# Kernel tuning notes

Hardware: AMD Instinct MI355X
Metric: run time of the kernel (lower is better)

## Reference

```python
import jax, jax.numpy as jnp
import numpy as np

N, E, IN, H, G = 50000, 800000, 200, 128, 512
L, M = 2, 2
D = H - 1  # Lorentz space dims
EPS = 1e-5


def _l_inner(x, y):
    return -x[..., :1] * y[..., :1] + jnp.sum(x[..., 1:] * y[..., 1:], -1, keepdims=True)


def _proj(x, c):
    s = x[..., 1:]
    t = jnp.sqrt(c + jnp.sum(s * s, -1, keepdims=True))
    return jnp.concatenate([t, s], -1)


def _expmap0(v, c):
    u = v[..., 1:]
    n = jnp.maximum(jnp.linalg.norm(u, axis=-1, keepdims=True), 1e-9)
    sc = jnp.sqrt(c)
    return jnp.concatenate([sc * jnp.cosh(n / sc), sc * jnp.sinh(n / sc) * u / n], -1)


def _logmap0(x, c):
    y = x[..., 1:]
    yn = jnp.maximum(jnp.linalg.norm(y, axis=-1, keepdims=True), 1e-9)
    sc = jnp.sqrt(c)
    d = sc * jnp.arccosh(jnp.maximum(x[..., :1] / sc, 1.0 + EPS))
    return jnp.concatenate([jnp.zeros_like(d), d * y / yn], -1)


def _dist(x, y, c):
    inner = -x[..., 0] * y[..., 0] + jnp.sum(x[..., 1:] * y[..., 1:], -1)
    val = jnp.maximum(-inner / c, 1.0 + EPS)
    return jnp.sqrt(c) * jnp.arccosh(val)


def _hyp_linear(x, w, b, c):
    v = _logmap0(x, c)                      # [n, H], time comp = 0
    os = v[..., 1:] @ w.T + b               # [n, D]
    return _proj(_expmap0(jnp.concatenate([v[..., :1], os], -1), c), c)


def _hyp_act(x, c):
    v = _logmap0(x, c)
    vs = jnp.tanh(v[..., 1:])
    return _expmap0(jnp.concatenate([jnp.zeros_like(v[..., :1]), vs], -1), c)


def _centroid(att, x, src, dst, c):
    # sparse weighted sum: m[i] = sum_{(i,j) in E} att_ij * x[j], then Lorentz normalize
    m = jax.ops.segment_sum(att[:, None] * x[dst], src, num_segments=N)
    denom = jnp.sqrt(jnp.maximum(-_l_inner(m, m), 1e-9))
    return jnp.sqrt(c) * m / denom


def _gin_layer(h, src, dst, aw, ab, eps, mw, mb, c):
    # distance-based attention on linearly transformed features
    hl = _hyp_linear(h, aw, ab, c)
    att = jnp.exp(-_dist(hl[src], hl[dst], c))   # [E]
    agg = _proj(_centroid(att, h, src, dst, c), c)
    hp = _proj(h, c)
    v = _logmap0(agg, c) + (1.0 + eps) * _logmap0(hp, c)
    out = _proj(_expmap0(v, c), c)
    for m in range(M):
        out = _hyp_act(_hyp_linear(out, mw[m], mb[m], c), c)
    return out


def setup_inputs() -> dict:
    key = jax.random.key(0)
    ks = jax.random.split(key, 8)
    x = jax.random.normal(ks[0], (N, IN), jnp.float32) * 0.1
    w_in = jax.random.normal(ks[1], (IN, D), jnp.float32) * (1.0 / np.sqrt(IN))
    att_w = jax.random.normal(ks[2], (L, D, D), jnp.float32) * (1.0 / np.sqrt(D))
    att_b = jnp.zeros((L, D), jnp.float32)
    mlp_w = jax.random.normal(ks[3], (L, M, D, D), jnp.float32) * (1.0 / np.sqrt(D))
    mlp_b = jnp.zeros((L, M, D), jnp.float32)
    eps = jnp.full((L,), 0.1, jnp.float32)
    c = jnp.ones((1,), jnp.float32)
    edge_index = jax.random.randint(ks[4], (2, E), 0, N)
    batch = jnp.sort(jax.random.randint(ks[5], (N,), 0, G))
    return {"x": x, "c": c, "w_in": w_in, "att_w": att_w, "att_b": att_b,
            "eps": eps, "mlp_w": mlp_w, "mlp_b": mlp_b,
            "edge_index": edge_index, "batch": batch}


def reference(x, c, w_in, att_w, att_b, eps, mlp_w, mlp_b, edge_index, batch):
    cc = c[0]
    src, dst = edge_index[0], edge_index[1]
    # Euclidean input proj -> tangent vector at origin -> manifold
    v0 = jnp.concatenate([jnp.zeros((x.shape[0], 1), x.dtype), x @ w_in], -1)
    h = _proj(_expmap0(v0, cc), cc)
    pooled = []
    for l in range(L):
        h = _gin_layer(h, src, dst, att_w[l], att_b[l], eps[l], mlp_w[l], mlp_b[l], cc)
        pooled.append(jax.ops.segment_sum(_logmap0(h, cc), batch, num_segments=G))
    return jnp.concatenate(pooled, -1)  # [G, L*H]
```

## Files before the change

kernel.cpp:

```cpp
#include <hip/hip_runtime.h>
#include <math.h>

#define NN 50000
#define NNP 50048
#define EE 800000
#define IN_F 200
#define DD 127
#define GG 512
#define EPSH 1e-5f

typedef unsigned int u32;
typedef unsigned short u16;
typedef __attribute__((ext_vector_type(8))) short short8;
typedef __attribute__((ext_vector_type(4))) float f32x4;

__device__ __forceinline__ u32 bf16r(float x) {
  u32 u = __float_as_uint(x);
  return (u + 0x7fffu + ((u >> 16) & 1u)) >> 16;
}

__device__ __forceinline__ u32 packhl(float v) {
  u32 hi = bf16r(v);
  float vh = __uint_as_float(hi << 16);
  u32 lo = bf16r(v - vh);
  return hi | (lo << 16);
}

__device__ __forceinline__ float rec(u32 u) {
  return __uint_as_float(u << 16) + __uint_as_float(u & 0xffff0000u);
}

#define WF_TOT (28672 + 6 * 16384)
__global__ void k_prep_wf(const float* __restrict__ att_w, const float* __restrict__ mlp_w,
                          const float* __restrict__ w_in, u16* __restrict__ Wfh,
                          u16* __restrict__ Wfl) {
  for (int idx = blockIdx.x * 256 + threadIdx.x; idx < WF_TOT; idx += gridDim.x * 256) {
    float val;
    if (idx < 28672) {
      int q = idx >> 12, rem = idx & 4095;
      int t = rem >> 9, l = (rem >> 3) & 63, j = rem & 7;
      int k = q * 32 + ((l >> 4) << 3) + j, n = t * 16 + (l & 15);
      val = (k < IN_F && n < DD) ? w_in[k * DD + n] : 0.f;
    } else {
      int rel = idx - 28672;
      int mat = rel >> 14, rem = rel & 16383;
      int q = rem >> 12;
      rem &= 4095;
      int t = rem >> 9, l = (rem >> 3) & 63, j = rem & 7;
      int k = q * 32 + ((l >> 4) << 3) + j, n = t * 16 + (l & 15);
      const float* wsrc = (mat < 2) ? att_w + mat * DD * DD : mlp_w + (mat - 2) * DD * DD;
      val = (k < DD && n < DD) ? wsrc[n * DD + k] : 0.f;
    }
    u32 hi = bf16r(val);
    float vh = __uint_as_float(hi << 16);
    u32 lo = bf16r(val - vh);
    Wfh[idx] = (u16)hi;
    Wfl[idx] = (u16)lo;
  }
}

__global__ void k_count(const int* __restrict__ idx, int n, int* __restrict__ cnt) {
  int i = blockIdx.x * blockDim.x + threadIdx.x;
  if (i < n) atomicAdd(&cnt[idx[i]], 1);
}

__global__ __launch_bounds__(1024) void k_scan_excl(const int* __restrict__ in, int n,
                                                    int* __restrict__ out, int* __restrict__ cur) {
  __shared__ int wbase[16];
  __shared__ int chunk_tot;
  int tid = threadIdx.x;
  int lane = tid & 63;
  int w = tid >> 6;
  int carry = 0;
  for (int base = 0; base < n; base += 4096) {
    int i0 = base + tid * 4;
    int v[4];
#pragma unroll
    for (int j = 0; j < 4; j++) v[j] = (i0 + j < n) ? in[i0 + j] : 0;
    int x = v[0] + v[1] + v[2] + v[3];
    int incl = x;
#pragma unroll
    for (int off = 1; off < 64; off <<= 1) {
      int t = __shfl_up(incl, off);
      if (lane >= off) incl += t;
    }
    if (lane == 63) wbase[w] = incl;
    __syncthreads();
    if (w == 0) {
      int t = (lane < 16) ? wbase[lane] : 0;
      int it = t;
#pragma unroll
      for (int off = 1; off < 16; off <<= 1) {
        int v2 = __shfl_up(it, off);
        if (lane >= off) it += v2;
      }
      if (lane < 16) wbase[lane] = it - t;
      if (lane == 15) chunk_tot = it;
    }
    __syncthreads();
    int run = carry + wbase[w] + (incl - x);
#pragma unroll
    for (int j = 0; j < 4; j++) {
      if (i0 + j < n) {
        out[i0 + j] = run;
        if (cur) cur[i0 + j] = run;
      }
      run += v[j];
    }
    carry += chunk_tot;
    __syncthreads();
  }
  if (tid == 0) out[n] = carry;
}

__global__ void k_scatter(const int* __restrict__ src, const int* __restrict__ dst, int n,
                          int* __restrict__ cursor, int* __restrict__ dst_sorted) {
  int e = blockIdx.x * blockDim.x + threadIdx.x;
  if (e < n) {
    int s = src[e];
    int slot = atomicAdd(&cursor[s], 1);
    dst_sorted[slot] = dst[e];
  }
}

__global__ void k_gptr(const int* __restrict__ batch, int* __restrict__ gptr) {
  int g = blockIdx.x * blockDim.x + threadIdx.x;
  if (g > GG) return;
  int lo = 0, hi = NN;
  while (lo < hi) {
    int mid = (lo + hi) >> 1;
    if (batch[mid] < g) lo = mid + 1; else hi = mid;
  }
  gptr[g] = lo;
}

#define MF_TANH 1
#define MF_T 2
#define MF_P 4

__device__ __forceinline__ void afrag_from_f32(const float* xv, u32* ahw, u32* alw) {
#pragma unroll
  for (int p = 0; p < 4; p++) {
    u32 h0 = bf16r(xv[2 * p]), h1 = bf16r(xv[2 * p + 1]);
    float f0 = __uint_as_float(h0 << 16), f1 = __uint_as_float(h1 << 16);
    ahw[p] = h0 | (h1 << 16);
    alw[p] = bf16r(xv[2 * p] - f0) | (bf16r(xv[2 * p + 1] - f1) << 16);
  }
}

template <int MODE>
__device__ __forceinline__ void epilogue(f32x4* acc, const float* __restrict__ bias,
                                         u32* __restrict__ To, u32* __restrict__ Pb,
                                         float* __restrict__ Pt, const float* __restrict__ cptr,
                                         int m0, int quad, int ml, int M) {
  float bj[8];
#pragma unroll
  for (int t = 0; t < 8; t++) {
    int col = t * 16 + ml;
    bj[t] = (bias != nullptr && col < DD) ? bias[col] : 0.f;
  }
  float cc = 1.f, sc = 1.f;
  if (MODE & MF_P) {
    cc = *cptr;
    sc = sqrtf(cc);
  }
#pragma unroll
  for (int r = 0; r < 4; r++) {
    int rowD = m0 + quad * 4 + r;
    float vs[8];
#pragma unroll
    for (int t = 0; t < 8; t++) {
      float v = acc[t][r] + bj[t];
      if (MODE & MF_TANH) {
        float e = exp2f(v * 2.8853900817779268f);
        v = 1.f - 2.f / (e + 1.f);
      }
      vs[t] = v;
    }
    if ((MODE & MF_T) && rowD < M) {
      u32* to = To + (size_t)rowD * 128 + ml;
#pragma unroll
      for (int t = 0; t < 8; t++) to[t * 16] = packhl(vs[t]);
    }
    if (MODE & MF_P) {
      float ps = 0.f;
#pragma unroll
      for (int t = 0; t < 8; t++) ps += vs[t] * vs[t];
#pragma unroll
      for (int off = 1; off < 16; off <<= 1) ps += __shfl_xor(ps, off);
      float nn = fmaxf(sqrtf(ps), 1e-9f);
      float e = expf(nn / sc);
      float f = sc * (e - 1.f / e) * 0.5f / nn;
      float tt = sqrtf(cc + f * f * ps);
      if (rowD < M) {
        u32* pb = Pb + (size_t)rowD * 128 + ml;
#pragma unroll
        for (int t = 0; t < 4; t++)
          pb[t * 16] = bf16r(f * vs[t]) | (bf16r(f * vs[t + 4]) << 16);
        if (ml == 0) Pt[rowD * 2] = tt;
      }
    }
  }
}

template <int MODE, int AF32>
__global__ __launch_bounds__(256) void k_mgemm(const float* __restrict__ Af,
                                               const u32* __restrict__ A32,
                                               const u16* __restrict__ Wfh,
                                               const u16* __restrict__ Wfl,
                                               const float* __restrict__ bias,
                                               u32* __restrict__ To, u32* __restrict__ Pb,
                                               float* __restrict__ Pt,
                                               const float* __restrict__ cptr, int M) {
  constexpr int NCH = AF32 ? 7 : 4;
  int lane = threadIdx.x & 63, wid = threadIdx.x >> 6;
  int m0 = blockIdx.x * 64 + wid * 16;
  int ml = lane & 15;
  int mld = m0 + ml;
  int quad = lane >> 4;
  f32x4 acc[8];
#pragma unroll
  for (int t = 0; t < 8; t++) acc[t] = (f32x4){0.f, 0.f, 0.f, 0.f};
#pragma unroll
  for (int q = 0; q < NCH; q++) {
    int k0 = q * 32 + quad * 8;
    union {
      short8 v;
      u32 w[4];
    } ah, al;
    if (AF32) {
      bool ok = (mld < M) && (k0 + 7 < IN_F);
      const float* ap = Af + (size_t)mld * IN_F + k0;
      float4 x0 = ok ? *(const float4*)ap : make_float4(0.f, 0.f, 0.f, 0.f);
      float4 x1 = ok ? *(const float4*)(ap + 4) : make_float4(0.f, 0.f, 0.f, 0.f);
      float xv[8] = {x0.x, x0.y, x0.z, x0.w, x1.x, x1.y, x1.z, x1.w};
      afrag_from_f32(xv, ah.w, al.w);
    } else {
      const u32* ap = A32 + (size_t)mld * 128 + k0;
      uint4 u0 = *(const uint4*)ap;
      uint4 u1 = *(const uint4*)(ap + 4);
      u32 uu[8] = {u0.x, u0.y, u0.z, u0.w, u1.x, u1.y, u1.z, u1.w};
#pragma unroll
      for (int p = 0; p < 4; p++) {
        ah.w[p] = __builtin_amdgcn_perm(uu[2 * p + 1], uu[2 * p], 0x05040100u);
        al.w[p] = __builtin_amdgcn_perm(uu[2 * p + 1], uu[2 * p], 0x07060302u);
      }
    }
    const u16* bph = Wfh + ((size_t)(q * 8) * 64 + lane) * 8;
    const u16* bpl = Wfl + ((size_t)(q * 8) * 64 + lane) * 8;
#pragma unroll
    for (int t = 0; t < 8; t++) {
      short8 bh = *(const short8*)(bph + t * 512);
      short8 bl = *(const short8*)(bpl + t * 512);
      acc[t] = __builtin_amdgcn_mfma_f32_16x16x32_bf16(ah.v, bh, acc[t], 0, 0, 0);
      acc[t] = __builtin_amdgcn_mfma_f32_16x16x32_bf16(al.v, bh, acc[t], 0, 0, 0);
      acc[t] = __builtin_amdgcn_mfma_f32_16x16x32_bf16(ah.v, bl, acc[t], 0, 0, 0);
    }
  }
  epilogue<MODE>(acc, bias, To, Pb, Pt, cptr, m0, quad, ml, M);
}

template <int MODE>
__global__ __launch_bounds__(256) void k_mgemm_mlp(const u32* __restrict__ A32,
                                                   const u16* __restrict__ Wha,
                                                   const u16* __restrict__ Wla,
                                                   const float* __restrict__ ba,
                                                   const u16* __restrict__ Whb,
                                                   const u16* __restrict__ Wlb,
                                                   const float* __restrict__ bb,
                                                   u32* __restrict__ To, u32* __restrict__ Pb,
                                                   float* __restrict__ Pt,
                                                   const float* __restrict__ cptr, int M) {
  __shared__ float tile[4][16][129];
  int lane = threadIdx.x & 63, wid = threadIdx.x >> 6;
  int m0 = blockIdx.x * 64 + wid * 16;
  int ml = lane & 15;
  int mld = m0 + ml;
  int quad = lane >> 4;
  f32x4 acc[8];
#pragma unroll
  for (int t = 0; t < 8; t++) acc[t] = (f32x4){0.f, 0.f, 0.f, 0.f};
#pragma unroll
  for (int q = 0; q < 4; q++) {
    int k0 = q * 32 + quad * 8;
    union {
      short8 v;
      u32 w[4];
    } ah, al;
    const u32* ap = A32 + (size_t)mld * 128 + k0;
    uint4 u0 = *(const uint4*)ap;
    uint4 u1 = *(const uint4*)(ap + 4);
    u32 uu[8] = {u0.x, u0.y, u0.z, u0.w, u1.x, u1.y, u1.z, u1.w};
#pragma unroll
    for (int p = 0; p < 4; p++) {
      ah.w[p] = __builtin_amdgcn_perm(uu[2 * p + 1], uu[2 * p], 0x05040100u);
      al.w[p] = __builtin_amdgcn_perm(uu[2 * p + 1], uu[2 * p], 0x07060302u);
    }
    const u16* bph = Wha + ((size_t)(q * 8) * 64 + lane) * 8;
    const u16* bpl = Wla + ((size_t)(q * 8) * 64 + lane) * 8;
#pragma unroll
    for (int t = 0; t < 8; t++) {
      short8 bh = *(const short8*)(bph + t * 512);
      short8 bl = *(const short8*)(bpl + t * 512);
      acc[t] = __builtin_amdgcn_mfma_f32_16x16x32_bf16(ah.v, bh, acc[t], 0, 0, 0);
      acc[t] = __builtin_amdgcn_mfma_f32_16x16x32_bf16(al.v, bh, acc[t], 0, 0, 0);
      acc[t] = __builtin_amdgcn_mfma_f32_16x16x32_bf16(ah.v, bl, acc[t], 0, 0, 0);
    }
  }
  {
    float bj[8];
#pragma unroll
    for (int t = 0; t < 8; t++) {
      int col = t * 16 + ml;
      bj[t] = (col < DD) ? ba[col] : 0.f;
    }
#pragma unroll
    for (int r = 0; r < 4; r++) {
#pragma unroll
      for (int t = 0; t < 8; t++) {
        float v = acc[t][r] + bj[t];
        float e = exp2f(v * 2.8853900817779268f);
        v = 1.f - 2.f / (e + 1.f);
        tile[wid][quad * 4 + r][t * 16 + ml] = v;
      }
    }
  }
  __syncthreads();
#pragma unroll
  for (int t = 0; t < 8; t++) acc[t] = (f32x4){0.f, 0.f, 0.f, 0.f};
#pragma unroll
  for (int q = 0; q < 4; q++) {
    int k0 = q * 32 + quad * 8;
    float xv[8];
#pragma unroll
    for (int j = 0; j < 8; j++) xv[j] = tile[wid][ml][k0 + j];
    union {
      short8 v;
      u32 w[4];
    } ah, al;
    afrag_from_f32(xv, ah.w, al.w);
    const u16* bph = Whb + ((size_t)(q * 8) * 64 + lane) * 8;
    const u16* bpl = Wlb + ((size_t)(q * 8) * 64 + lane) * 8;
#pragma unroll
    for (int t = 0; t < 8; t++) {
      short8 bh = *(const short8*)(bph + t * 512);
      short8 bl = *(const short8*)(bpl + t * 512);
      acc[t] = __builtin_amdgcn_mfma_f32_16x16x32_bf16(ah.v, bh, acc[t], 0, 0, 0);
      acc[t] = __builtin_amdgcn_mfma_f32_16x16x32_bf16(al.v, bh, acc[t], 0, 0, 0);
      acc[t] = __builtin_amdgcn_mfma_f32_16x16x32_bf16(ah.v, bl, acc[t], 0, 0, 0);
    }
  }
  epilogue<MODE>(acc, bb, To, Pb, Pt, cptr, m0, quad, ml, M);
}

__global__ void k_agg_q(const u32* __restrict__ HHb, const float2* __restrict__ ptHH,
                        const u32* __restrict__ T, const int* __restrict__ rowp,
                        const int* __restrict__ dsts, const float* __restrict__ epsp,
                        const float* __restrict__ cptr, u32* __restrict__ Tout, int n) {
  int node = blockIdx.x * 4 + (threadIdx.x >> 6);
  int lane = threadIdx.x & 63;
  if (node >= n) return;
  int p = lane & 15;
  int q = lane >> 4;
  float c = *cptr, sc = sqrtf(c), rcpc = 1.f / c;
  float eps = *epsp;
  uint4 a4 = *(const uint4*)(HHb + (size_t)node * 128 + p * 4);
  float alo[4], ahi[4];
  {
    u32 aw[4] = {a4.x, a4.y, a4.z, a4.w};
#pragma unroll
    for (int j = 0; j < 4; j++) {
      alo[j] = __uint_as_float(aw[j] << 16);
      ahi[j] = __uint_as_float(aw[j] & 0xffff0000u);
    }
  }
  float pts = ptHH[node].x;
  int e0 = rowp[node], e1 = rowp[node + 1];
  int iters = (e1 - e0 + 3) >> 2;
  float m[8] = {0.f, 0.f, 0.f, 0.f, 0.f, 0.f, 0.f, 0.f};
  float mt = 0.f;
#pragma unroll 2
  for (int it = 0; it < iters; it++) {
    int e = e0 + it * 4 + q;
    bool ve = e < e1;
    int ei = ve ? e : e0;
    int d = dsts[ei];
    const u32* rb = HHb + (size_t)d * 128 + p * 4;
    uint4 b4 = *(const uint4*)rb;
    uint4 h4 = *(const uint4*)(rb + 64);
    float2 pp = ptHH[d];
    u32 bw[4] = {b4.x, b4.y, b4.z, b4.w};
    float dot = 0.f;
#pragma unroll
    for (int j = 0; j < 4; j++) {
      dot = fmaf(alo[j], __uint_as_float(bw[j] << 16), dot);
      dot = fmaf(ahi[j], __uint_as_float(bw[j] & 0xffff0000u), dot);
    }
#pragma unroll
    for (int off = 1; off < 16; off <<= 1) dot += __shfl_xor(dot, off);
    float valv = fmaxf((pts * pp.x - dot) * rcpc, 1.f + EPSH);
    float w = valv + sqrtf(fmaf(valv, valv, -1.f));
    float att = exp2f(-sc * __log2f(w));
    att = ve ? att : 0.f;
    u32 hw[4] = {h4.x, h4.y, h4.z, h4.w};
#pragma unroll
    for (int j = 0; j < 4; j++) {
      m[j] = fmaf(att, __uint_as_float(hw[j] << 16), m[j]);
      m[4 + j] = fmaf(att, __uint_as_float(hw[j] & 0xffff0000u), m[4 + j]);
    }
    mt = fmaf(att, pp.y, mt);
  }
#pragma unroll
  for (int j = 0; j < 8; j++) {
    m[j] += __shfl_xor(m[j], 16);
    m[j] += __shfl_xor(m[j], 32);
  }
  mt += __shfl_xor(mt, 16);
  mt += __shfl_xor(mt, 32);
  float lp = 0.f;
#pragma unroll
  for (int j = 0; j < 8; j++) lp = fmaf(m[j], m[j], lp);
#pragma unroll
  for (int off = 1; off < 16; off <<= 1) lp += __shfl_xor(lp, off);
  float lsq = lp;
  float neg_inner = mt * mt - lsq;
  float denom = sqrtf(fmaxf(neg_inner, 1e-9f));
  float r = sc / denom;
  float ssq = r * r * lsq;
  float agg0 = sqrtf(c + ssq);
  float ynA = fmaxf(sqrtf(ssq), 1e-9f);
  float v2 = fmaxf(agg0 / sc, 1.f + EPSH);
  float dA = sc * 0.69314718056f * __log2f(v2 + sqrtf(v2 * v2 - 1.f));
  float sca = dA * r / ynA;
  uint4 t0 = *(const uint4*)(T + (size_t)node * 128 + p * 4);
  uint4 t1 = *(const uint4*)(T + (size_t)node * 128 + 64 + p * 4);
  u32 tw0[4] = {t0.x, t0.y, t0.z, t0.w};
  u32 tw1[4] = {t1.x, t1.y, t1.z, t1.w};
  float oe = 1.f + eps;
  uint4 o0, o1;
  u32* po0 = (u32*)&o0;
  u32* po1 = (u32*)&o1;
#pragma unroll
  for (int j = 0; j < 4; j++) {
    po0[j] = packhl(fmaf(sca, m[j], oe * rec(tw0[j])));
    po1[j] = packhl(fmaf(sca, m[4 + j], oe * rec(tw1[j])));
  }
  if (q == 0) {
    *(uint4*)(Tout + (size_t)node * 128 + p * 4) = o0;
    *(uint4*)(Tout + (size_t)node * 128 + 64 + p * 4) = o1;
  }
}

__global__ void k_pool(const u32* __restrict__ U, const int* __restrict__ gptr,
                       float* __restrict__ out, int layer) {
  int g = blockIdx.x;
  int c = threadIdx.x;
  int s = gptr[g], e = gptr[g + 1];
  float acc = 0.f;
  if (c > 0) {
    const u32* up = U + (c - 1);
    int i = s;
    float a0 = 0.f, a1 = 0.f, a2 = 0.f, a3 = 0.f;
    for (; i + 3 < e; i += 4) {
      a0 += rec(up[(size_t)i * 128]);
      a1 += rec(up[(size_t)(i + 1) * 128]);
      a2 += rec(up[(size_t)(i + 2) * 128]);
      a3 += rec(up[(size_t)(i + 3) * 128]);
    }
    for (; i < e; i++) a0 += rec(up[(size_t)i * 128]);
    acc = (a0 + a1) + (a2 + a3);
  }
  out[(size_t)g * 256 + layer * 128 + c] = acc;
}

extern "C" void kernel_launch(void* const* d_in, const int* in_sizes, int n_in, void* d_out,
                              int out_size, void* d_ws, size_t ws_size, hipStream_t stream) {
  const float* x = (const float*)d_in[0];
  const float* cptr = (const float*)d_in[1];
  const float* w_in = (const float*)d_in[2];
  const float* att_w = (const float*)d_in[3];
  const float* att_b = (const float*)d_in[4];
  const float* epsv = (const float*)d_in[5];
  const float* mlp_w = (const float*)d_in[6];
  const float* mlp_b = (const float*)d_in[7];
  const int* ei = (const int*)d_in[8];
  const int* batch = (const int*)d_in[9];
  const int* srcp = ei;
  const int* dstp = ei + EE;
  float* out = (float*)d_out;

  u32* ws = (u32*)d_ws;
  u16* Wfh = (u16*)ws;
  u16* Wfl = Wfh + WF_TOT;
  int* deg = (int*)(ws + 126976);
  int* rowp = deg + NN;
  int* cursor = rowp + NN + 1;
  int* gptr = cursor + NN;
  int* dsts = gptr + GG + 1;
  size_t o1 = (size_t)((u32*)(dsts + EE) - ws);
  o1 = (o1 + 3) & ~(size_t)3;
  float2* ptHH = (float2*)(ws + o1);
  u32* HHb = ws + o1 + 2 * NNP;
  u32* A32 = HHb + (size_t)NNP * 128;
  u32* B32 = A32 + (size_t)NNP * 128;

  const int EW = 12500;
  const int GEMMG = (NN + 63) / 64;

  hipMemsetAsync(deg, 0, NN * sizeof(int), stream);
  k_prep_wf<<<64, 256, 0, stream>>>(att_w, mlp_w, w_in, Wfh, Wfl);
  k_count<<<(EE + 255) / 256, 256, 0, stream>>>(srcp, EE, deg);
  k_gptr<<<3, 256, 0, stream>>>(batch, gptr);
  k_scan_excl<<<1, 1024, 0, stream>>>(deg, NN, rowp, cursor);
  k_scatter<<<(EE + 255) / 256, 256, 0, stream>>>(srcp, dstp, EE, cursor, dsts);

#define WH(m) (Wfh + 28672 + (m) * 16384)
#define WL(m) (Wfl + 28672 + (m) * 16384)
  float* ptX = (float*)ptHH;

  k_mgemm<MF_T | MF_P, 1><<<GEMMG, 256, 0, stream>>>(x, nullptr, Wfh, Wfl, nullptr, A32,
                                                     HHb + 64, ptX + 1, cptr, NN);

  k_mgemm<MF_P, 0><<<GEMMG, 256, 0, stream>>>(nullptr, A32, WH(0), WL(0), att_b, nullptr, HHb,
                                              ptX, cptr, NN);
  k_agg_q<<<EW, 256, 0, stream>>>(HHb, ptHH, A32, rowp, dsts, epsv + 0, cptr, B32, NN);
  k_mgemm_mlp<MF_TANH | MF_T | MF_P><<<GEMMG, 256, 0, stream>>>(
      B32, WH(2), WL(2), mlp_b + 0 * DD, WH(3), WL(3), mlp_b + 1 * DD, A32, HHb + 64, ptX + 1,
      cptr, NN);
  k_pool<<<GG, 128, 0, stream>>>(A32, gptr, out, 0);

  k_mgemm<MF_P, 0><<<GEMMG, 256, 0, stream>>>(nullptr, A32, WH(1), WL(1), att_b + DD, nullptr,
                                              HHb, ptX, cptr, NN);
  k_agg_q<<<EW, 256, 0, stream>>>(HHb, ptHH, A32, rowp, dsts, epsv + 1, cptr, B32, NN);
  k_mgemm_mlp<MF_TANH | MF_T><<<GEMMG, 256, 0, stream>>>(B32, WH(4), WL(4), mlp_b + 2 * DD,
                                                         WH(5), WL(5), mlp_b + 3 * DD, B32,
                                                         nullptr, nullptr, cptr, NN);
  k_pool<<<GG, 128, 0, stream>>>(B32, gptr, out, 1);
}
```

Before: 547.0 us.

## Fuse attention GEMM into preceding kernels and use fp16 packed edge aggregation

Folds the attention hyperbolic-linear GEMM into the input-projection kernel and into the MLP kernel, passing activations through shared memory. This removes two standalone GEMM launches and their re-read of the activations. The edge aggregation now stores the per-node features as fp16 pairs (scaled by 1/64 to limit overflow) instead of bf16. It computes dot products with packed fdot2, accumulates with packed half FMAs, and assigns 8 lanes per edge with 8 edges in flight per wave. Accumulating in fp16 risks precision loss and overflow on high-degree nodes.

```diff
diff --git a/kernel.cpp b/kernel.cpp
--- a/kernel.cpp
+++ b/kernel.cpp
@@ -1,4 +1,5 @@
 #include <hip/hip_runtime.h>
+#include <hip/hip_fp16.h>
 #include <math.h>
 
 #define NN 50000
@@ -8,11 +9,19 @@
 #define DD 127
 #define GG 512
 #define EPSH 1e-5f
+#define PS_SCALE 0.015625f
 
 typedef unsigned int u32;
 typedef unsigned short u16;
 typedef __attribute__((ext_vector_type(8))) short short8;
 typedef __attribute__((ext_vector_type(4))) float f32x4;
+typedef _Float16 h2f __attribute__((ext_vector_type(2)));
+typedef __fp16 fp16x2 __attribute__((ext_vector_type(2)));
+union UH {
+  u32 u;
+  h2f h;
+  fp16x2 f;
+};
 
 __device__ __forceinline__ u32 bf16r(float x) {
   u32 u = __float_as_uint(x);
@@ -28,6 +37,29 @@
 
 __device__ __forceinline__ float rec(u32 u) {
   return __uint_as_float(u << 16) + __uint_as_float(u & 0xffff0000u);
+}
+
+__device__ __forceinline__ u32 pk2h(float a, float b) {
+#if __has_builtin(__builtin_amdgcn_cvt_pkrtz)
+  UH x;
+  x.f = __builtin_amdgcn_cvt_pkrtz(a, b);
+  return x.u;
+#else
+  __half2 r = __floats2half2_rn(a, b);
+  return *(u32*)&r;
+#endif
+}
+
+__device__ __forceinline__ float fdot2h(u32 a, u32 b, float acc) {
+  UH ua, ub;
+  ua.u = a;
+  ub.u = b;
+#if __has_builtin(__builtin_amdgcn_fdot2)
+  return __builtin_amdgcn_fdot2(ua.h, ub.h, acc, false);
+#else
+  acc = fmaf((float)ua.h[0], (float)ub.h[0], acc);
+  return fmaf((float)ua.h[1], (float)ub.h[1], acc);
+#endif
 }
 
 #define WF_TOT (28672 + 6 * 16384)
@@ -134,294 +166,327 @@
   gptr[g] = lo;
 }
 
-#define MF_TANH 1
-#define MF_T 2
-#define MF_P 4
-
-__device__ __forceinline__ void afrag_from_f32(const float* xv, u32* ahw, u32* alw) {
+union AB {
+  short8 v;
+  u32 w[4];
+};
+
+__device__ __forceinline__ void build_hl(const float* xv, AB& ah, AB& al) {
 #pragma unroll
   for (int p = 0; p < 4; p++) {
     u32 h0 = bf16r(xv[2 * p]), h1 = bf16r(xv[2 * p + 1]);
     float f0 = __uint_as_float(h0 << 16), f1 = __uint_as_float(h1 << 16);
-    ahw[p] = h0 | (h1 << 16);
-    alw[p] = bf16r(xv[2 * p] - f0) | (bf16r(xv[2 * p + 1] - f1) << 16);
-  }
-}
-
-template <int MODE>
-__device__ __forceinline__ void epilogue(f32x4* acc, const float* __restrict__ bias,
-                                         u32* __restrict__ To, u32* __restrict__ Pb,
-                                         float* __restrict__ Pt, const float* __restrict__ cptr,
-                                         int m0, int quad, int ml, int M) {
-  float bj[8];
+    ah.w[p] = h0 | (h1 << 16);
+    al.w[p] = bf16r(xv[2 * p] - f0) | (bf16r(xv[2 * p + 1] - f1) << 16);
+  }
+}
+
+__device__ __forceinline__ void mfma3(const AB& ah, const AB& al, const u16* __restrict__ Wh,
+                                      const u16* __restrict__ Wl, int q, int lane, f32x4* acc) {
+  const u16* bph = Wh + ((size_t)(q * 8) * 64 + lane) * 8;
+  const u16* bpl = Wl + ((size_t)(q * 8) * 64 + lane) * 8;
 #pragma unroll
   for (int t = 0; t < 8; t++) {
-    int col = t * 16 + ml;
-    bj[t] = (bias != nullptr && col < DD) ? bias[col] : 0.f;
-  }
-  float cc = 1.f, sc = 1.f;
-  if (MODE & MF_P) {
-    cc = *cptr;
-    sc = sqrtf(cc);
-  }
-#pragma unroll
-  for (int r = 0; r < 4; r++) {
-    int rowD = m0 + quad * 4 + r;
-    float vs[8];
-#pragma unroll
-    for (int t = 0; t < 8; t++) {
-      float v = acc[t][r] + bj[t];
-      if (MODE & MF_TANH) {
-        float e = exp2f(v * 2.8853900817779268f);
-        v = 1.f - 2.f / (e + 1.f);
-      }
-      vs[t] = v;
-    }
-    if ((MODE & MF_T) && rowD < M) {
-      u32* to = To + (size_t)rowD * 128 + ml;
-#pragma unroll
-      for (int t = 0; t < 8; t++) to[t * 16] = packhl(vs[t]);
-    }
-    if (MODE & MF_P) {
-      float ps = 0.f;
-#pragma unroll
-      for (int t = 0; t < 8; t++) ps += vs[t] * vs[t];
-#pragma unroll
-      for (int off = 1; off < 16; off <<= 1) ps += __shfl_xor(ps, off);
-      float nn = fmaxf(sqrtf(ps), 1e-9f);
-      float e = expf(nn / sc);
-      float f = sc * (e - 1.f / e) * 0.5f / nn;
-      float tt = sqrtf(cc + f * f * ps);
-      if (rowD < M) {
-        u32* pb = Pb + (size_t)rowD * 128 + ml;
-#pragma unroll
-        for (int t = 0; t < 4; t++)
-          pb[t * 16] = bf16r(f * vs[t]) | (bf16r(f * vs[t + 4]) << 16);
-        if (ml == 0) Pt[rowD * 2] = tt;
-      }
-    }
-  }
-}
-
-template <int MODE, int AF32>
-__global__ __launch_bounds__(256) void k_mgemm(const float* __restrict__ Af,
-                                               const u32* __restrict__ A32,
-                                               const u16* __restrict__ Wfh,
-                                               const u16* __restrict__ Wfl,
-                                               const float* __restrict__ bias,
-                                               u32* __restrict__ To, u32* __restrict__ Pb,
-                                               float* __restrict__ Pt,
-                                               const float* __restrict__ cptr, int M) {
-  constexpr int NCH = AF32 ? 7 : 4;
-  int lane = threadIdx.x & 63, wid = threadIdx.x >> 6;
-  int m0 = blockIdx.x * 64 + wid * 16;
-  int ml = lane & 15;
-  int mld = m0 + ml;
-  int quad = lane >> 4;
-  f32x4 acc[8];
-#pragma unroll
-  for (int t = 0; t < 8; t++) acc[t] = (f32x4){0.f, 0.f, 0.f, 0.f};
-#pragma unroll
-  for (int q = 0; q < NCH; q++) {
-    int k0 = q * 32 + quad * 8;
-    union {
-      short8 v;
-      u32 w[4];
-    } ah, al;
-    if (AF32) {
-      bool ok = (mld < M) && (k0 + 7 < IN_F);
-      const float* ap = Af + (size_t)mld * IN_F + k0;
-      float4 x0 = ok ? *(const float4*)ap : make_float4(0.f, 0.f, 0.f, 0.f);
-      float4 x1 = ok ? *(const float4*)(ap + 4) : make_float4(0.f, 0.f, 0.f, 0.f);
-      float xv[8] = {x0.x, x0.y, x0.z, x0.w, x1.x, x1.y, x1.z, x1.w};
-      afrag_from_f32(xv, ah.w, al.w);
-    } else {
-      const u32* ap = A32 + (size_t)mld * 128 + k0;
-      uint4 u0 = *(const uint4*)ap;
-      uint4 u1 = *(const uint4*)(ap + 4);
-      u32 uu[8] = {u0.x, u0.y, u0.z, u0.w, u1.x, u1.y, u1.z, u1.w};
-#pragma unroll
-      for (int p = 0; p < 4; p++) {
-        ah.w[p] = __builtin_amdgcn_perm(uu[2 * p + 1], uu[2 * p], 0x05040100u);
-        al.w[p] = __builtin_amdgcn_perm(uu[2 * p + 1], uu[2 * p], 0x07060302u);
-      }
-    }
-    const u16* bph = Wfh + ((size_t)(q * 8) * 64 + lane) * 8;
-    const u16* bpl = Wfl + ((size_t)(q * 8) * 64 + lane) * 8;
-#pragma unroll
-    for (int t = 0; t < 8; t++) {
-      short8 bh = *(const short8*)(bph + t * 512);
-      short8 bl = *(const short8*)(bpl + t * 512);
-      acc[t] = __builtin_amdgcn_mfma_f32_16x16x32_bf16(ah.v, bh, acc[t], 0, 0, 0);
-      acc[t] = __builtin_amdgcn_mfma_f32_16x16x32_bf16(al.v, bh, acc[t], 0, 0, 0);
-      acc[t] = __builtin_amdgcn_mfma_f32_16x16x32_bf16(ah.v, bl, acc[t], 0, 0, 0);
-    }
-  }
-  epilogue<MODE>(acc, bias, To, Pb, Pt, cptr, m0, quad, ml, M);
-}
-
-template <int MODE>
-__global__ __launch_bounds__(256) void k_mgemm_mlp(const u32* __restrict__ A32,
-                                                   const u16* __restrict__ Wha,
-                                                   const u16* __restrict__ Wla,
-                                                   const float* __restrict__ ba,
-                                                   const u16* __restrict__ Whb,
-                                                   const u16* __restrict__ Wlb,
-                                                   const float* __restrict__ bb,
-                                                   u32* __restrict__ To, u32* __restrict__ Pb,
-                                                   float* __restrict__ Pt,
-                                                   const float* __restrict__ cptr, int M) {
-  __shared__ float tile[4][16][129];
-  int lane = threadIdx.x & 63, wid = threadIdx.x >> 6;
-  int m0 = blockIdx.x * 64 + wid * 16;
-  int ml = lane & 15;
-  int mld = m0 + ml;
-  int quad = lane >> 4;
-  f32x4 acc[8];
-#pragma unroll
-  for (int t = 0; t < 8; t++) acc[t] = (f32x4){0.f, 0.f, 0.f, 0.f};
+    short8 bh = *(const short8*)(bph + t * 512);
+    short8 bl = *(const short8*)(bpl + t * 512);
+    acc[t] = __builtin_amdgcn_mfma_f32_16x16x32_bf16(ah.v, bh, acc[t], 0, 0, 0);
+    acc[t] = __builtin_amdgcn_mfma_f32_16x16x32_bf16(al.v, bh, acc[t], 0, 0, 0);
+    acc[t] = __builtin_amdgcn_mfma_f32_16x16x32_bf16(ah.v, bl, acc[t], 0, 0, 0);
+  }
+}
+
+__device__ __forceinline__ void gemm_packhl(const u32* __restrict__ A32, int mld,
+                                            const u16* __restrict__ Wh,
+                                            const u16* __restrict__ Wl, int lane, int quad,
+                                            f32x4* acc) {
 #pragma unroll
   for (int q = 0; q < 4; q++) {
     int k0 = q * 32 + quad * 8;
-    union {
-      short8 v;
-      u32 w[4];
-    } ah, al;
     const u32* ap = A32 + (size_t)mld * 128 + k0;
     uint4 u0 = *(const uint4*)ap;
     uint4 u1 = *(const uint4*)(ap + 4);
     u32 uu[8] = {u0.x, u0.y, u0.z, u0.w, u1.x, u1.y, u1.z, u1.w};
+    AB ah, al;
 #pragma unroll
     for (int p = 0; p < 4; p++) {
       ah.w[p] = __builtin_amdgcn_perm(uu[2 * p + 1], uu[2 * p], 0x05040100u);
       al.w[p] = __builtin_amdgcn_perm(uu[2 * p + 1], uu[2 * p], 0x07060302u);
     }
-    const u16* bph = Wha + ((size_t)(q * 8) * 64 + lane) * 8;
-    const u16* bpl = Wla + ((size_t)(q * 8) * 64 + lane) * 8;
-#pragma unroll
-    for (int t = 0; t < 8; t++) {
-      short8 bh = *(const short8*)(bph + t * 512);
-      short8 bl = *(const short8*)(bpl + t * 512);
-      acc[t] = __builtin_amdgcn_mfma_f32_16x16x32_bf16(ah.v, bh, acc[t], 0, 0, 0);
-      acc[t] = __builtin_amdgcn_mfma_f32_16x16x32_bf16(al.v, bh, acc[t], 0, 0, 0);
-      acc[t] = __builtin_amdgcn_mfma_f32_16x16x32_bf16(ah.v, bl, acc[t], 0, 0, 0);
-    }
-  }
-  {
-    float bj[8];
-#pragma unroll
-    for (int t = 0; t < 8; t++) {
-      int col = t * 16 + ml;
-      bj[t] = (col < DD) ? ba[col] : 0.f;
-    }
-#pragma unroll
-    for (int r = 0; r < 4; r++) {
-#pragma unroll
-      for (int t = 0; t < 8; t++) {
-        float v = acc[t][r] + bj[t];
-        float e = exp2f(v * 2.8853900817779268f);
-        v = 1.f - 2.f / (e + 1.f);
-        tile[wid][quad * 4 + r][t * 16 + ml] = v;
-      }
-    }
-  }
-  __syncthreads();
-#pragma unroll
-  for (int t = 0; t < 8; t++) acc[t] = (f32x4){0.f, 0.f, 0.f, 0.f};
+    mfma3(ah, al, Wh, Wl, q, lane, acc);
+  }
+}
+
+__device__ __forceinline__ void gemm_lds(const float (*tile)[129], int ml, int quad, int lane,
+                                         const u16* __restrict__ Wh, const u16* __restrict__ Wl,
+                                         f32x4* acc) {
 #pragma unroll
   for (int q = 0; q < 4; q++) {
     int k0 = q * 32 + quad * 8;
     float xv[8];
 #pragma unroll
-    for (int j = 0; j < 8; j++) xv[j] = tile[wid][ml][k0 + j];
-    union {
-      short8 v;
-      u32 w[4];
-    } ah, al;
-    afrag_from_f32(xv, ah.w, al.w);
-    const u16* bph = Whb + ((size_t)(q * 8) * 64 + lane) * 8;
-    const u16* bpl = Wlb + ((size_t)(q * 8) * 64 + lane) * 8;
-#pragma unroll
-    for (int t = 0; t < 8; t++) {
-      short8 bh = *(const short8*)(bph + t * 512);
-      short8 bl = *(const short8*)(bpl + t * 512);
-      acc[t] = __builtin_amdgcn_mfma_f32_16x16x32_bf16(ah.v, bh, acc[t], 0, 0, 0);
-      acc[t] = __builtin_amdgcn_mfma_f32_16x16x32_bf16(al.v, bh, acc[t], 0, 0, 0);
-      acc[t] = __builtin_amdgcn_mfma_f32_16x16x32_bf16(ah.v, bl, acc[t], 0, 0, 0);
-    }
-  }
-  epilogue<MODE>(acc, bb, To, Pb, Pt, cptr, m0, quad, ml, M);
-}
-
-__global__ void k_agg_q(const u32* __restrict__ HHb, const float2* __restrict__ ptHH,
-                        const u32* __restrict__ T, const int* __restrict__ rowp,
-                        const int* __restrict__ dsts, const float* __restrict__ epsp,
-                        const float* __restrict__ cptr, u32* __restrict__ Tout, int n) {
+    for (int j = 0; j < 8; j++) xv[j] = tile[ml][k0 + j];
+    AB ah, al;
+    build_hl(xv, ah, al);
+    mfma3(ah, al, Wh, Wl, q, lane, acc);
+  }
+}
+
+__device__ __forceinline__ void bias8(const float* __restrict__ bias, int ml, float* bj) {
+#pragma unroll
+  for (int t = 0; t < 8; t++) {
+    int col = t * 16 + ml;
+    bj[t] = (bias != nullptr && col < DD) ? bias[col] : 0.f;
+  }
+}
+
+template <int TANH>
+__device__ __forceinline__ void row_vs(const f32x4* acc, const float* bj, int r, float* vs) {
+#pragma unroll
+  for (int t = 0; t < 8; t++) {
+    float v = acc[t][r] + bj[t];
+    if (TANH) {
+      float e = exp2f(v * 2.8853900817779268f);
+      v = 1.f - 2.f / (e + 1.f);
+    }
+    vs[t] = v;
+  }
+}
+
+__device__ __forceinline__ void store_T_row(const float* vs, u32* __restrict__ To, int rowD,
+                                            int ml) {
+  u32* to = To + (size_t)rowD * 128 + ml;
+#pragma unroll
+  for (int t = 0; t < 8; t++) to[t * 16] = packhl(vs[t]);
+}
+
+__device__ __forceinline__ void store_P_row(const float* vs, u32* __restrict__ Pb,
+                                            float* __restrict__ Pt, int rowD, int ml, float cc,
+                                            float sc, float pscale) {
+  float ps = 0.f;
+#pragma unroll
+  for (int t = 0; t < 8; t++) ps += vs[t] * vs[t];
+#pragma unroll
+  for (int off = 1; off < 16; off <<= 1) ps += __shfl_xor(ps, off);
+  float nn = fmaxf(sqrtf(ps), 1e-9f);
+  float e = expf(nn / sc);
+  float f = sc * (e - 1.f / e) * 0.5f / nn;
+  float tt = sqrtf(cc + f * f * ps);
+  f *= pscale;
+  u32* pb = Pb + (size_t)rowD * 128 + ml;
+#pragma unroll
+  for (int t = 0; t < 4; t++) pb[t * 16] = pk2h(f * vs[t], f * vs[t + 4]);
+  if (ml == 0) Pt[rowD * 2] = pscale * tt;
+}
+
+__global__ __launch_bounds__(256) void k_gemm_in(
+    const float* __restrict__ x, const u16* __restrict__ WhI, const u16* __restrict__ WlI,
+    const u16* __restrict__ WhA, const u16* __restrict__ WlA, const float* __restrict__ attb,
+    u32* __restrict__ To, u32* __restrict__ HHh, float* __restrict__ ptF,
+    const float* __restrict__ cptr, int M) {
+  __shared__ float tile[4][16][129];
+  int lane = threadIdx.x & 63, wid = threadIdx.x >> 6;
+  int m0 = blockIdx.x * 64 + wid * 16;
+  int ml = lane & 15, quad = lane >> 4;
+  int mld = m0 + ml;
+  f32x4 acc[8];
+#pragma unroll
+  for (int t = 0; t < 8; t++) acc[t] = (f32x4){0.f, 0.f, 0.f, 0.f};
+#pragma unroll
+  for (int q = 0; q < 7; q++) {
+    int k0 = q * 32 + quad * 8;
+    bool ok = (mld < M) && (k0 + 7 < IN_F);
+    const float* ap = x + (size_t)mld * IN_F + k0;
+    float4 x0 = ok ? *(const float4*)ap : make_float4(0.f, 0.f, 0.f, 0.f);
+    float4 x1 = ok ? *(const float4*)(ap + 4) : make_float4(0.f, 0.f, 0.f, 0.f);
+    float xv[8] = {x0.x, x0.y, x0.z, x0.w, x1.x, x1.y, x1.z, x1.w};
+    AB ah, al;
+    build_hl(xv, ah, al);
+    mfma3(ah, al, WhI, WlI, q, lane, acc);
+  }
+  float cc = *cptr, sc = sqrtf(cc);
+  {
+    float bj[8];
+    bias8(nullptr, ml, bj);
+#pragma unroll
+    for (int r = 0; r < 4; r++) {
+      int rowD = m0 + quad * 4 + r;
+      float vs[8];
+      row_vs<0>(acc, bj, r, vs);
+      if (rowD < M) {
+        store_T_row(vs, To, rowD, ml);
+        store_P_row(vs, HHh + 64, ptF + 1, rowD, ml, cc, sc, PS_SCALE);
+      }
+#pragma unroll
+      for (int t = 0; t < 8; t++) tile[wid][quad * 4 + r][t * 16 + ml] = vs[t];
+    }
+  }
+#pragma unroll
+  for (int t = 0; t < 8; t++) acc[t] = (f32x4){0.f, 0.f, 0.f, 0.f};
+  gemm_lds(tile[wid], ml, quad, lane, WhA, WlA, acc);
+  {
+    float bj[8];
+    bias8(attb, ml, bj);
+#pragma unroll
+    for (int r = 0; r < 4; r++) {
+      int rowD = m0 + quad * 4 + r;
+      float vs[8];
+      row_vs<0>(acc, bj, r, vs);
+      if (rowD < M) store_P_row(vs, HHh, ptF, rowD, ml, cc, sc, 1.f);
+    }
+  }
+}
+
+template <int LAST>
+__global__ __launch_bounds__(256) void k_mlp3(
+    const u32* __restrict__ A32, const u16* __restrict__ Wha, const u16* __restrict__ Wla,
+    const float* __restrict__ ba, const u16* __restrict__ Whb, const u16* __restrict__ Wlb,
+    const float* __restrict__ bb, const u16* __restrict__ WhA, const u16* __restrict__ WlA,
+    const float* __restrict__ attb, u32* __restrict__ To, u32* __restrict__ HHh,
+    float* __restrict__ ptF, const float* __restrict__ cptr, int M) {
+  __shared__ float tile[4][16][129];
+  int lane = threadIdx.x & 63, wid = threadIdx.x >> 6;
+  int m0 = blockIdx.x * 64 + wid * 16;
+  int ml = lane & 15, quad = lane >> 4;
+  int mld = m0 + ml;
+  f32x4 acc[8];
+#pragma unroll
+  for (int t = 0; t < 8; t++) acc[t] = (f32x4){0.f, 0.f, 0.f, 0.f};
+  gemm_packhl(A32, mld, Wha, Wla, lane, quad, acc);
+  {
+    float bj[8];
+    bias8(ba, ml, bj);
+#pragma unroll
+    for (int r = 0; r < 4; r++) {
+      float vs[8];
+      row_vs<1>(acc, bj, r, vs);
+#pragma unroll
+      for (int t = 0; t < 8; t++) tile[wid][quad * 4 + r][t * 16 + ml] = vs[t];
+    }
+  }
+#pragma unroll
+  for (int t = 0; t < 8; t++) acc[t] = (f32x4){0.f, 0.f, 0.f, 0.f};
+  gemm_lds(tile[wid], ml, quad, lane, Whb, Wlb, acc);
+  float cc = 1.f, sc = 1.f;
+  if (!LAST) {
+    cc = *cptr;
+    sc = sqrtf(cc);
+  }
+  {
+    float bj[8];
+    bias8(bb, ml, bj);
+#pragma unroll
+    for (int r = 0; r < 4; r++) {
+      int rowD = m0 + quad * 4 + r;
+      float vs[8];
+      row_vs<1>(acc, bj, r, vs);
+      if (rowD < M) store_T_row(vs, To, rowD, ml);
+      if (!LAST) {
+        if (rowD < M) store_P_row(vs, HHh + 64, ptF + 1, rowD, ml, cc, sc, PS_SCALE);
+#pragma unroll
+        for (int t = 0; t < 8; t++) tile[wid][quad * 4 + r][t * 16 + ml] = vs[t];
+      }
+    }
+  }
+  if (!LAST) {
+#pragma unroll
+    for (int t = 0; t < 8; t++) acc[t] = (f32x4){0.f, 0.f, 0.f, 0.f};
+    gemm_lds(tile[wid], ml, quad, lane, WhA, WlA, acc);
+    float bj[8];
+    bias8(attb, ml, bj);
+#pragma unroll
+    for (int r = 0; r < 4; r++) {
+      int rowD = m0 + quad * 4 + r;
+      float vs[8];
+      row_vs<0>(acc, bj, r, vs);
+      if (rowD < M) store_P_row(vs, HHh, ptF, rowD, ml, cc, sc, 1.f);
+    }
+  }
+}
+
+__global__ __launch_bounds__(256) void k_agg_o(const u32* __restrict__ HHh,
+                                               const float2* __restrict__ ptHH,
+                                               const u32* __restrict__ T,
+                                               const int* __restrict__ rowp,
+                                               const int* __restrict__ dsts,
+                                               const float* __restrict__ epsp,
+                                               const float* __restrict__ cptr,
+                                               u32* __restrict__ Tout, int n) {
   int node = blockIdx.x * 4 + (threadIdx.x >> 6);
   int lane = threadIdx.x & 63;
   if (node >= n) return;
-  int p = lane & 15;
-  int q = lane >> 4;
+  int o = lane & 7, g = lane >> 3;
   float c = *cptr, sc = sqrtf(c), rcpc = 1.f / c;
   float eps = *epsp;
-  uint4 a4 = *(const uint4*)(HHb + (size_t)node * 128 + p * 4);
-  float alo[4], ahi[4];
-  {
-    u32 aw[4] = {a4.x, a4.y, a4.z, a4.w};
-#pragma unroll
-    for (int j = 0; j < 4; j++) {
-      alo[j] = __uint_as_float(aw[j] << 16);
-      ahi[j] = __uint_as_float(aw[j] & 0xffff0000u);
-    }
-  }
+  const u32* arow = HHh + (size_t)node * 128 + o * 8;
+  uint4 a0 = *(const uint4*)arow;
+  uint4 a1 = *(const uint4*)(arow + 4);
+  u32 apk[8] = {a0.x, a0.y, a0.z, a0.w, a1.x, a1.y, a1.z, a1.w};
   float pts = ptHH[node].x;
   int e0 = rowp[node], e1 = rowp[node + 1];
-  int iters = (e1 - e0 + 3) >> 2;
-  float m[8] = {0.f, 0.f, 0.f, 0.f, 0.f, 0.f, 0.f, 0.f};
+  int iters = (e1 - e0 + 7) >> 3;
+  h2f mpk[8];
+  {
+    UH z;
+    z.u = 0;
+#pragma unroll
+    for (int j = 0; j < 8; j++) mpk[j] = z.h;
+  }
   float mt = 0.f;
 #pragma unroll 2
   for (int it = 0; it < iters; it++) {
-    int e = e0 + it * 4 + q;
+    int e = e0 + it * 8 + g;
     bool ve = e < e1;
-    int ei = ve ? e : e0;
-    int d = dsts[ei];
-    const u32* rb = HHb + (size_t)d * 128 + p * 4;
-    uint4 b4 = *(const uint4*)rb;
-    uint4 h4 = *(const uint4*)(rb + 64);
+    int d = dsts[ve ? e : e0];
+    const u32* rb = HHh + (size_t)d * 128 + o * 8;
+    uint4 b0 = *(const uint4*)rb;
+    uint4 b1 = *(const uint4*)(rb + 4);
+    uint4 h0 = *(const uint4*)(rb + 64);
+    uint4 h1 = *(const uint4*)(rb + 68);
     float2 pp = ptHH[d];
-    u32 bw[4] = {b4.x, b4.y, b4.z, b4.w};
+    u32 bw[8] = {b0.x, b0.y, b0.z, b0.w, b1.x, b1.y, b1.z, b1.w};
     float dot = 0.f;
 #pragma unroll
-    for (int j = 0; j < 4; j++) {
-      dot = fmaf(alo[j], __uint_as_float(bw[j] << 16), dot);
-      dot = fmaf(ahi[j], __uint_as_float(bw[j] & 0xffff0000u), dot);
-    }
-#pragma unroll
-    for (int off = 1; off < 16; off <<= 1) dot += __shfl_xor(dot, off);
+    for (int j = 0; j < 8; j++) dot = fdot2h(apk[j], bw[j], dot);
+    dot += __shfl_xor(dot, 1);
+    dot += __shfl_xor(dot, 2);
+    dot += __shfl_xor(dot, 4);
     float valv = fmaxf((pts * pp.x - dot) * rcpc, 1.f + EPSH);
     float w = valv + sqrtf(fmaf(valv, valv, -1.f));
     float att = exp2f(-sc * __log2f(w));
     att = ve ? att : 0.f;
-    u32 hw[4] = {h4.x, h4.y, h4.z, h4.w};
-#pragma unroll
-    for (int j = 0; j < 4; j++) {
-      m[j] = fmaf(att, __uint_as_float(hw[j] << 16), m[j]);
-      m[4 + j] = fmaf(att, __uint_as_float(hw[j] & 0xffff0000u), m[4 + j]);
+    UH att2;
+    att2.u = pk2h(att, att);
+    u32 hw[8] = {h0.x, h0.y, h0.z, h0.w, h1.x, h1.y, h1.z, h1.w};
+#pragma unroll
+    for (int j = 0; j < 8; j++) {
+      UH hv;
+      hv.u = hw[j];
+      mpk[j] = att2.h * hv.h + mpk[j];
     }
     mt = fmaf(att, pp.y, mt);
   }
 #pragma unroll
+  for (int off = 8; off <= 32; off <<= 1) {
+#pragma unroll
+    for (int j = 0; j < 8; j++) {
+      UH v;
+      v.h = mpk[j];
+      UH s;
+      s.u = (u32)__shfl_xor((int)v.u, off);
+      mpk[j] = v.h + s.h;
+    }
+    mt += __shfl_xor(mt, off);
+  }
+  float lp = 0.f;
+#pragma unroll
   for (int j = 0; j < 8; j++) {
-    m[j] += __shfl_xor(m[j], 16);
-    m[j] += __shfl_xor(m[j], 32);
-  }
-  mt += __shfl_xor(mt, 16);
-  mt += __shfl_xor(mt, 32);
-  float lp = 0.f;
-#pragma unroll
-  for (int j = 0; j < 8; j++) lp = fmaf(m[j], m[j], lp);
-#pragma unroll
-  for (int off = 1; off < 16; off <<= 1) lp += __shfl_xor(lp, off);
+    float lo = (float)mpk[j][0], hi = (float)mpk[j][1];
+    lp = fmaf(lo, lo, lp);
+    lp = fmaf(hi, hi, lp);
+  }
+  lp += __shfl_xor(lp, 1);
+  lp += __shfl_xor(lp, 2);
+  lp += __shfl_xor(lp, 4);
   float lsq = lp;
   float neg_inner = mt * mt - lsq;
   float denom = sqrtf(fmaxf(neg_inner, 1e-9f));
@@ -432,22 +497,27 @@
   float v2 = fmaxf(agg0 / sc, 1.f + EPSH);
   float dA = sc * 0.69314718056f * __log2f(v2 + sqrtf(v2 * v2 - 1.f));
   float sca = dA * r / ynA;
-  uint4 t0 = *(const uint4*)(T + (size_t)node * 128 + p * 4);
-  uint4 t1 = *(const uint4*)(T + (size_t)node * 128 + 64 + p * 4);
-  u32 tw0[4] = {t0.x, t0.y, t0.z, t0.w};
-  u32 tw1[4] = {t1.x, t1.y, t1.z, t1.w};
-  float oe = 1.f + eps;
-  uint4 o0, o1;
-  u32* po0 = (u32*)&o0;
-  u32* po1 = (u32*)&o1;
-#pragma unroll
-  for (int j = 0; j < 4; j++) {
-    po0[j] = packhl(fmaf(sca, m[j], oe * rec(tw0[j])));
-    po1[j] = packhl(fmaf(sca, m[4 + j], oe * rec(tw1[j])));
-  }
-  if (q == 0) {
-    *(uint4*)(Tout + (size_t)node * 128 + p * 4) = o0;
-    *(uint4*)(Tout + (size_t)node * 128 + 64 + p * 4) = o1;
+  if (g == 0) {
+    const u32* tp = T + (size_t)node * 128 + o * 8;
+    uint4 t0 = *(const uint4*)tp;
+    uint4 t0b = *(const uint4*)(tp + 4);
+    uint4 t1 = *(const uint4*)(tp + 64);
+    uint4 t1b = *(const uint4*)(tp + 68);
+    u32 tw[8] = {t0.x, t0.y, t0.z, t0.w, t0b.x, t0b.y, t0b.z, t0b.w};
+    u32 tv[8] = {t1.x, t1.y, t1.z, t1.w, t1b.x, t1b.y, t1b.z, t1b.w};
+    float oe = 1.f + eps;
+    u32 olo[8], ohi[8];
+#pragma unroll
+    for (int j = 0; j < 8; j++) {
+      float lo = (float)mpk[j][0], hi = (float)mpk[j][1];
+      olo[j] = packhl(fmaf(sca, lo, oe * rec(tw[j])));
+      ohi[j] = packhl(fmaf(sca, hi, oe * rec(tv[j])));
+    }
+    u32* op = Tout + (size_t)node * 128 + o * 8;
+    *(uint4*)op = make_uint4(olo[0], olo[1], olo[2], olo[3]);
+    *(uint4*)(op + 4) = make_uint4(olo[4], olo[5], olo[6], olo[7]);
+    *(uint4*)(op + 64) = make_uint4(ohi[0], ohi[1], ohi[2], ohi[3]);
+    *(uint4*)(op + 68) = make_uint4(ohi[4], ohi[5], ohi[6], ohi[7]);
   }
 }
 
@@ -500,14 +570,15 @@
   size_t o1 = (size_t)((u32*)(dsts + EE) - ws);
   o1 = (o1 + 3) & ~(size_t)3;
   float2* ptHH = (float2*)(ws + o1);
-  u32* HHb = ws + o1 + 2 * NNP;
-  u32* A32 = HHb + (size_t)NNP * 128;
+  u32* HHh = ws + o1 + 2 * NNP;
+  u32* A32 = HHh + (size_t)NNP * 128;
   u32* B32 = A32 + (size_t)NNP * 128;
 
   const int EW = 12500;
   const int GEMMG = (NN + 63) / 64;
-
-  hipMemsetAsync(deg, 0, NN * sizeof(int), stream);
+  float* ptF = (float*)ptHH;
+
+  (void)hipMemsetAsync(deg, 0, NN * sizeof(int), stream);
   k_prep_wf<<<64, 256, 0, stream>>>(att_w, mlp_w, w_in, Wfh, Wfl);
   k_count<<<(EE + 255) / 256, 256, 0, stream>>>(srcp, EE, deg);
   k_gptr<<<3, 256, 0, stream>>>(batch, gptr);
@@ -516,24 +587,18 @@
 
 #define WH(m) (Wfh + 28672 + (m) * 16384)
 #define WL(m) (Wfl + 28672 + (m) * 16384)
-  float* ptX = (float*)ptHH;
-
-  k_mgemm<MF_T | MF_P, 1><<<GEMMG, 256, 0, stream>>>(x, nullptr, Wfh, Wfl, nullptr, A32,
-                                                     HHb + 64, ptX + 1, cptr, NN);
-
-  k_mgemm<MF_P, 0><<<GEMMG, 256, 0, stream>>>(nullptr, A32, WH(0), WL(0), att_b, nullptr, HHb,
-                                              ptX, cptr, NN);
-  k_agg_q<<<EW, 256, 0, stream>>>(HHb, ptHH, A32, rowp, dsts, epsv + 0, cptr, B32, NN);
-  k_mgemm_mlp<MF_TANH | MF_T | MF_P><<<GEMMG, 256, 0, stream>>>(
-      B32, WH(2), WL(2), mlp_b + 0 * DD, WH(3), WL(3), mlp_b + 1 * DD, A32, HHb + 64, ptX + 1,
-      cptr, NN);
+
+  k_gemm_in<<<GEMMG, 256, 0, stream>>>(x, Wfh, Wfl, WH(0), WL(0), att_b, A32, HHh, ptF, cptr, NN);
+
+  k_agg_o<<<EW, 256, 0, stream>>>(HHh, ptHH, A32, rowp, dsts, epsv + 0, cptr, B32, NN);
+  k_mlp3<0><<<GEMMG, 256, 0, stream>>>(B32, WH(2), WL(2), mlp_b + 0 * DD, WH(3), WL(3),
+                                       mlp_b + 1 * DD, WH(1), WL(1), att_b + DD, A32, HHh, ptF,
+                                       cptr, NN);
   k_pool<<<GG, 128, 0, stream>>>(A32, gptr, out, 0);
 
-  k_mgemm<MF_P, 0><<<GEMMG, 256, 0, stream>>>(nullptr, A32, WH(1), WL(1), att_b + DD, nullptr,
-                                              HHb, ptX, cptr, NN);
-  k_agg_q<<<EW, 256, 0, stream>>>(HHb, ptHH, A32, rowp, dsts, epsv + 1, cptr, B32, NN);
-  k_mgemm_mlp<MF_TANH | MF_T><<<GEMMG, 256, 0, stream>>>(B32, WH(4), WL(4), mlp_b + 2 * DD,
-                                                         WH(5), WL(5), mlp_b + 3 * DD, B32,
-                                                         nullptr, nullptr, cptr, NN);
+  k_agg_o<<<EW, 256, 0, stream>>>(HHh, ptHH, A32, rowp, dsts, epsv + 1, cptr, B32, NN);
+  k_mlp3<1><<<GEMMG, 256, 0, stream>>>(B32, WH(4), WL(4), mlp_b + 2 * DD, WH(5), WL(5),
+                                       mlp_b + 3 * DD, nullptr, nullptr, nullptr, B32, nullptr,
+                                       nullptr, cptr, NN);
   k_pool<<<GG, 128, 0, stream>>>(B32, gptr, out, 1);
 }
```

Measured after the change: 522.1 us. 4.5% less time.
